# Kernel tuning notes

Hardware: AMD Instinct MI355X
Metric: run time of the kernel (lower is better)

## Reference

```python
import jax, jax.numpy as jnp
import numpy as np

B, T_IN, T_OUT, ADIM, PDIM, EDIM = 32, 512, 2048, 384, 4, 1


def setup_inputs() -> dict:
    key = jax.random.key(0)
    ks = jax.random.split(key, 8)
    hs = jax.random.normal(ks[0], (B, T_IN, ADIM), dtype=jnp.float32)
    # durations in [1, 5) so max expanded length 4*T_IN == T_OUT (no truncation)
    durations = jax.random.randint(ks[1], (B, T_IN), 1, 5).astype(jnp.int64)
    input_lengths = (T_IN // 2 + jax.random.randint(ks[2], (B,), 0, T_IN // 2)).astype(jnp.int64)
    pitch_target = jax.random.normal(ks[3], (B, T_OUT, PDIM), dtype=jnp.float32)
    energy_target = jax.random.normal(ks[4], (B, T_OUT, EDIM), dtype=jnp.float32)
    duration_mask = jnp.zeros((B, T_IN, 1), dtype=bool)
    variance_mask = jnp.zeros((B, T_OUT, 1), dtype=bool)
    # kernel-size-1 ConvNorm weights (kernel dim squeezed) + biases
    pitch_w = jax.random.normal(ks[5], (ADIM, PDIM), dtype=jnp.float32) / np.sqrt(PDIM)
    pitch_b = jnp.zeros((ADIM,), dtype=jnp.float32)
    energy_w = jax.random.normal(ks[6], (ADIM, EDIM), dtype=jnp.float32) / np.sqrt(EDIM)
    energy_b = jnp.zeros((ADIM,), dtype=jnp.float32)
    return dict(hs=hs, durations=durations, input_lengths=input_lengths,
                pitch_target=pitch_target, energy_target=energy_target,
                duration_mask=duration_mask, variance_mask=variance_mask,
                pitch_w=pitch_w, pitch_b=pitch_b, energy_w=energy_w, energy_b=energy_b)


def length_regulate(xs, durations, input_lengths, t_out):
    # xs: [B, T_in, D]; durations: [B, T_in]; output: [B, t_out, D], zero-padded
    Bsz, Tin, D = xs.shape
    pos = jnp.arange(Tin)
    valid = pos[None, :] < input_lengths[:, None]            # [B, T_in]
    d = jnp.where(valid, durations, 0)
    total = d.sum(axis=-1)
    # torch: if d.sum()==0, fill truncated d with ones
    d = jnp.where((total == 0)[:, None] & valid, 1, d)
    cum = jnp.cumsum(d, axis=-1)                             # [B, T_in]
    t = jnp.arange(t_out)
    # source phone index per output frame: count of cum entries <= t
    idx = jax.vmap(lambda c: jnp.searchsorted(c, t, side='right'))(cum)  # [B, t_out]
    idx = jnp.clip(idx, 0, Tin - 1)
    out = jnp.take_along_axis(xs, idx[..., None], axis=1)    # [B, t_out, D]
    frame_mask = t[None, :] < cum[:, -1:]                    # [B, t_out]
    return jnp.where(frame_mask[..., None], out, jnp.zeros((), xs.dtype))


def reference(hs, durations, input_lengths, pitch_target, energy_target,
              duration_mask, variance_mask, pitch_w, pitch_b, energy_w, energy_b):
    hs = length_regulate(hs, durations, input_lengths, T_OUT)      # [B, T_out, adim]
    # kernel-size-1 convs == pointwise linear over channel dim (dropout rate 0)
    pitch_embed = jnp.einsum('btp,ap->bta', pitch_target, pitch_w) + pitch_b
    energy_embed = jnp.einsum('bte,ae->bta', energy_target, energy_w) + energy_b
    return hs + pitch_embed + energy_embed
```

## Files before the change

kernel.cpp:

```cpp
#include <hip/hip_runtime.h>

constexpr int kB    = 32;
constexpr int kTin  = 512;
constexpr int kTout = 2048;
constexpr int kA    = 384;
constexpr int kC4   = kA / 4;

__global__ __launch_bounds__(kTin) void lr_index_kernel(
    const int* __restrict__ durations,
    const int* __restrict__ input_lengths,
    int* __restrict__ idx_out)
{
    __shared__ int cum[kTin];
    const int b = blockIdx.x;
    const int t = threadIdx.x;
    const int len = input_lengths[b];
    const bool valid = t < len;
    int dval = valid ? durations[b * kTin + t] : 0;
    int total = 0;
    for (int pass = 0; pass < 2; ++pass) {
        __syncthreads();
        cum[t] = dval;
        __syncthreads();
        for (int off = 1; off < kTin; off <<= 1) {
            int add = (t >= off) ? cum[t - off] : 0;
            __syncthreads();
            cum[t] += add;
            __syncthreads();
        }
        total = cum[kTin - 1];
        if (total != 0) break;
        dval = valid ? 1 : 0;
    }
    for (int k = 0; k < kTout / kTin; ++k) {
        const int to = t + k * kTin;
        int lo = 0, hi = kTin;
        while (lo < hi) {
            const int mid = (lo + hi) >> 1;
            if (cum[mid] <= to) lo = mid + 1; else hi = mid;
        }
        int idx = (lo < kTin) ? lo : (kTin - 1);
        idx_out[b * kTout + to] = (to < total) ? idx : -1;
    }
}

__global__ __launch_bounds__(384) void fuse_kernel(
    const float*  __restrict__ hs,
    const int*    __restrict__ idx,
    const float4* __restrict__ pitch_t,
    const float*  __restrict__ energy_t,
    const float4* __restrict__ pitch_w,
    const float*  __restrict__ pitch_b,
    const float*  __restrict__ energy_w,
    const float*  __restrict__ energy_b,
    float4*       __restrict__ out)
{
    const int tid = threadIdx.x;
    const int c4  = tid % kC4;
    const int sub = tid / kC4;
    const int a0  = c4 * 4;

    const float4 w0 = pitch_w[a0];
    const float4 w1 = pitch_w[a0 + 1];
    const float4 w2 = pitch_w[a0 + 2];
    const float4 w3 = pitch_w[a0 + 3];
    const float4 ew = make_float4(energy_w[a0], energy_w[a0 + 1],
                                  energy_w[a0 + 2], energy_w[a0 + 3]);
    const float4 bias = make_float4(pitch_b[a0]     + energy_b[a0],
                                    pitch_b[a0 + 1] + energy_b[a0 + 1],
                                    pitch_b[a0 + 2] + energy_b[a0 + 2],
                                    pitch_b[a0 + 3] + energy_b[a0 + 3]);

    const long nrows = (long)kB * kTout;
    for (long row = (long)blockIdx.x * 4 + sub; row < nrows;
         row += 4L * gridDim.x) {
        const int src = idx[row];
        float4 h = make_float4(0.f, 0.f, 0.f, 0.f);
        if (src >= 0) {
            const long b = row >> 11;
            h = *(const float4*)(hs + (b * kTin + src) * (long)kA + a0);
        }
        const float4 pt = pitch_t[row];
        const float  e  = energy_t[row];
        float4 o;
        o.x = h.x + pt.x * w0.x + pt.y * w0.y + pt.z * w0.z + pt.w * w0.w + e * ew.x + bias.x;
        o.y = h.y + pt.x * w1.x + pt.y * w1.y + pt.z * w1.z + pt.w * w1.w + e * ew.y + bias.y;
        o.z = h.z + pt.x * w2.x + pt.y * w2.y + pt.z * w2.z + pt.w * w2.w + e * ew.z + bias.z;
        o.w = h.w + pt.x * w3.x + pt.y * w3.y + pt.z * w3.z + pt.w * w3.w + e * ew.w + bias.w;
        out[row * kC4 + c4] = o;
    }
}

extern "C" void kernel_launch(void* const* d_in, const int* in_sizes, int n_in,
                              void* d_out, int out_size, void* d_ws, size_t ws_size,
                              hipStream_t stream) {
    const float* hs            = (const float*)d_in[0];
    const int*   durations     = (const int*)d_in[1];
    const int*   input_lengths = (const int*)d_in[2];
    const float* pitch_t       = (const float*)d_in[3];
    const float* energy_t      = (const float*)d_in[4];
    const float* pitch_w       = (const float*)d_in[7];
    const float* pitch_b       = (const float*)d_in[8];
    const float* energy_w      = (const float*)d_in[9];
    const float* energy_b      = (const float*)d_in[10];
    float* out = (float*)d_out;
    int*   idx = (int*)d_ws;

    lr_index_kernel<<<kB, kTin, 0, stream>>>(durations, input_lengths, idx);
    fuse_kernel<<<1024, 384, 0, stream>>>(hs, idx,
        (const float4*)pitch_t, energy_t,
        (const float4*)pitch_w, pitch_b, energy_w, energy_b,
        (float4*)out);
}
```

Measured before the change: 158.4 us.

## Fuse length-regulation index computation into the output kernel per batch slice

Merges the two kernels into one. Each block recomputes the duration prefix sum for its batch in shared memory, using double buffering, then binary-searches source indices inline. This removes the second launch and the idx workspace round-trip. The cost is redundant scans (16 blocks per batch each redo the same scan), a per-row binary search inside every thread, and a smaller grid of 512 blocks. Output writes also switch to nontemporal stores.

```diff
diff --git a/kernel.cpp b/kernel.cpp
--- a/kernel.cpp
+++ b/kernel.cpp
@@ -6,88 +6,107 @@
 constexpr int kA    = 384;
 constexpr int kC4   = kA / 4;
 
-__global__ __launch_bounds__(kTin) void lr_index_kernel(
-    const int* __restrict__ durations,
-    const int* __restrict__ input_lengths,
-    int* __restrict__ idx_out)
+constexpr int kBlocksPerBatch = 16;
+constexpr int kRowsPerBlock   = kTout / kBlocksPerBatch;
+
+typedef float v4f __attribute__((ext_vector_type(4)));
+
+__global__ __launch_bounds__(384) void va_fused_kernel(
+    const float* __restrict__ hs,
+    const int*   __restrict__ durations,
+    const int*   __restrict__ input_lengths,
+    const v4f*   __restrict__ pitch_t,
+    const float* __restrict__ energy_t,
+    const v4f*   __restrict__ pitch_w,
+    const float* __restrict__ pitch_b,
+    const float* __restrict__ energy_w,
+    const float* __restrict__ energy_b,
+    v4f*         __restrict__ out)
 {
-    __shared__ int cum[kTin];
-    const int b = blockIdx.x;
-    const int t = threadIdx.x;
+    __shared__ int bufA[kTin];
+    __shared__ int bufB[kTin];
+
+    const int tid = threadIdx.x;
+    const int b   = blockIdx.x >> 4;
+    const int blk = blockIdx.x & 15;
     const int len = input_lengths[b];
-    const bool valid = t < len;
-    int dval = valid ? durations[b * kTin + t] : 0;
-    int total = 0;
-    for (int pass = 0; pass < 2; ++pass) {
+
+    for (int i = tid; i < kTin; i += 384)
+        bufA[i] = (i < len) ? durations[b * kTin + i] : 0;
+    __syncthreads();
+    int* scur = bufA;
+    int* snxt = bufB;
+    for (int off = 1; off < kTin; off <<= 1) {
+        for (int i = tid; i < kTin; i += 384) {
+            int v = scur[i];
+            if (i >= off) v += scur[i - off];
+            snxt[i] = v;
+        }
         __syncthreads();
-        cum[t] = dval;
+        int* t = scur; scur = snxt; snxt = t;
+    }
+    int total = scur[kTin - 1];
+    if (total == 0) {
+        __syncthreads();
+        for (int i = tid; i < kTin; i += 384)
+            scur[i] = (i < len) ? 1 : 0;
         __syncthreads();
         for (int off = 1; off < kTin; off <<= 1) {
-            int add = (t >= off) ? cum[t - off] : 0;
+            for (int i = tid; i < kTin; i += 384) {
+                int v = scur[i];
+                if (i >= off) v += scur[i - off];
+                snxt[i] = v;
+            }
             __syncthreads();
-            cum[t] += add;
-            __syncthreads();
+            int* t = scur; scur = snxt; snxt = t;
         }
-        total = cum[kTin - 1];
-        if (total != 0) break;
-        dval = valid ? 1 : 0;
+        total = scur[kTin - 1];
     }
-    for (int k = 0; k < kTout / kTin; ++k) {
-        const int to = t + k * kTin;
-        int lo = 0, hi = kTin;
-        while (lo < hi) {
-            const int mid = (lo + hi) >> 1;
-            if (cum[mid] <= to) lo = mid + 1; else hi = mid;
-        }
-        int idx = (lo < kTin) ? lo : (kTin - 1);
-        idx_out[b * kTout + to] = (to < total) ? idx : -1;
-    }
-}
+    const int* __restrict__ cum = scur;
 
-__global__ __launch_bounds__(384) void fuse_kernel(
-    const float*  __restrict__ hs,
-    const int*    __restrict__ idx,
-    const float4* __restrict__ pitch_t,
-    const float*  __restrict__ energy_t,
-    const float4* __restrict__ pitch_w,
-    const float*  __restrict__ pitch_b,
-    const float*  __restrict__ energy_w,
-    const float*  __restrict__ energy_b,
-    float4*       __restrict__ out)
-{
-    const int tid = threadIdx.x;
     const int c4  = tid % kC4;
     const int sub = tid / kC4;
     const int a0  = c4 * 4;
 
-    const float4 w0 = pitch_w[a0];
-    const float4 w1 = pitch_w[a0 + 1];
-    const float4 w2 = pitch_w[a0 + 2];
-    const float4 w3 = pitch_w[a0 + 3];
-    const float4 ew = make_float4(energy_w[a0], energy_w[a0 + 1],
-                                  energy_w[a0 + 2], energy_w[a0 + 3]);
-    const float4 bias = make_float4(pitch_b[a0]     + energy_b[a0],
-                                    pitch_b[a0 + 1] + energy_b[a0 + 1],
-                                    pitch_b[a0 + 2] + energy_b[a0 + 2],
-                                    pitch_b[a0 + 3] + energy_b[a0 + 3]);
+    const v4f w0 = pitch_w[a0];
+    const v4f w1 = pitch_w[a0 + 1];
+    const v4f w2 = pitch_w[a0 + 2];
+    const v4f w3 = pitch_w[a0 + 3];
+    v4f ew;
+    ew.x = energy_w[a0];     ew.y = energy_w[a0 + 1];
+    ew.z = energy_w[a0 + 2]; ew.w = energy_w[a0 + 3];
+    v4f bias;
+    bias.x = pitch_b[a0]     + energy_b[a0];
+    bias.y = pitch_b[a0 + 1] + energy_b[a0 + 1];
+    bias.z = pitch_b[a0 + 2] + energy_b[a0 + 2];
+    bias.w = pitch_b[a0 + 3] + energy_b[a0 + 3];
 
-    const long nrows = (long)kB * kTout;
-    for (long row = (long)blockIdx.x * 4 + sub; row < nrows;
-         row += 4L * gridDim.x) {
-        const int src = idx[row];
-        float4 h = make_float4(0.f, 0.f, 0.f, 0.f);
-        if (src >= 0) {
-            const long b = row >> 11;
-            h = *(const float4*)(hs + (b * kTin + src) * (long)kA + a0);
+    const int row0 = blk * kRowsPerBlock;
+    const int hs_base = b * kTin * kA;
+    const int row_base = b * kTout;
+
+    for (int r = sub; r < kRowsPerBlock; r += 4) {
+        const int to  = row0 + r;
+        const int row = row_base + to;
+
+        v4f h = (v4f)(0.f);
+        if (to < total) {
+            int lo = 0, hi = kTin;
+            while (lo < hi) {
+                const int mid = (lo + hi) >> 1;
+                if (cum[mid] <= to) lo = mid + 1; else hi = mid;
+            }
+            const int sidx = (lo < kTin) ? lo : (kTin - 1);
+            h = *(const v4f*)(hs + hs_base + sidx * kA + a0);
         }
-        const float4 pt = pitch_t[row];
-        const float  e  = energy_t[row];
-        float4 o;
+        const v4f  pt = pitch_t[row];
+        const float e = energy_t[row];
+        v4f o;
         o.x = h.x + pt.x * w0.x + pt.y * w0.y + pt.z * w0.z + pt.w * w0.w + e * ew.x + bias.x;
         o.y = h.y + pt.x * w1.x + pt.y * w1.y + pt.z * w1.z + pt.w * w1.w + e * ew.y + bias.y;
         o.z = h.z + pt.x * w2.x + pt.y * w2.y + pt.z * w2.z + pt.w * w2.w + e * ew.z + bias.z;
         o.w = h.w + pt.x * w3.x + pt.y * w3.y + pt.z * w3.z + pt.w * w3.w + e * ew.w + bias.w;
-        out[row * kC4 + c4] = o;
+        __builtin_nontemporal_store(o, &out[row * kC4 + c4]);
     }
 }
 
@@ -104,11 +123,10 @@
     const float* energy_w      = (const float*)d_in[9];
     const float* energy_b      = (const float*)d_in[10];
     float* out = (float*)d_out;
-    int*   idx = (int*)d_ws;
 
-    lr_index_kernel<<<kB, kTin, 0, stream>>>(durations, input_lengths, idx);
-    fuse_kernel<<<1024, 384, 0, stream>>>(hs, idx,
-        (const float4*)pitch_t, energy_t,
-        (const float4*)pitch_w, pitch_b, energy_w, energy_b,
-        (float4*)out);
+    va_fused_kernel<<<kB * kBlocksPerBatch, 384, 0, stream>>>(
+        hs, durations, input_lengths,
+        (const v4f*)pitch_t, energy_t,
+        (const v4f*)pitch_w, pitch_b, energy_w, energy_b,
+        (v4f*)out);
 }
```

Measured after the change: 176.9 us. 11.7% more time.
